# Optimization experiments

Hardware: AMD Instinct MI355X
Metric: run time of the kernel (lower is better)

Reference implementation:

```python
import jax, jax.numpy as jnp
import numpy as np

N = 100000
E = 1600000
E_PAIR = 100000
D_IN = 128
D_H = 128


def _sage_mean(x, src, dst, W_neigh, W_self, b):
    # DGL SAGEConv('mean'): out = fc_self(h_dst) + fc_neigh(mean_{u in N(v)} h_u) + bias
    n = x.shape[0]
    msg_sum = jax.ops.segment_sum(x[src], dst, num_segments=n)          # [N, d]
    deg = jax.ops.segment_sum(jnp.ones(src.shape, x.dtype), dst, num_segments=n)
    h_neigh = msg_sum / jnp.maximum(deg, 1.0)[:, None]
    return x @ W_self.T + h_neigh @ W_neigh.T + b


def setup_inputs() -> dict:
    key = jax.random.key(0)
    ks = jax.random.split(key, 16)
    def lin(k, fan_out, fan_in):
        s = 1.0 / np.sqrt(fan_in)
        return jax.random.uniform(k, (fan_out, fan_in), jnp.float32, -s, s)
    inp = {
        'x': jax.random.normal(ks[0], (N, D_IN), jnp.float32),
        'edge_src': jax.random.randint(ks[1], (E,), 0, N),
        'edge_dst': jax.random.randint(ks[2], (E,), 0, N),
        'pos_src': jax.random.randint(ks[3], (E_PAIR,), 0, N),
        'pos_dst': jax.random.randint(ks[4], (E_PAIR,), 0, N),
        'neg_src': jax.random.randint(ks[5], (E_PAIR,), 0, N),
        'neg_dst': jax.random.randint(ks[6], (E_PAIR,), 0, N),
        # SAGEConv layer 1 (in_feats -> n_hidden)
        'W1_neigh': lin(ks[7], D_H, D_IN),
        'W1_self': lin(ks[8], D_H, D_IN),
        'b1': jnp.zeros((D_H,), jnp.float32),
        # SAGEConv layer 2 (n_hidden -> n_hidden)
        'W2_neigh': lin(ks[9], D_H, D_H),
        'W2_self': lin(ks[10], D_H, D_H),
        'b2': jnp.zeros((D_H,), jnp.float32),
        # predictor MLP: Linear(2h->h) ReLU Linear(h->h) ReLU Linear(h->1)
        'P1_w': lin(ks[11], D_H, 2 * D_H),
        'P1_b': jnp.zeros((D_H,), jnp.float32),
        'P2_w': lin(ks[12], D_H, D_H),
        'P2_b': jnp.zeros((D_H,), jnp.float32),
        'P3_w': lin(ks[13], 1, D_H),
        'P3_b': jnp.zeros((1,), jnp.float32),
    }
    return inp


def _predict(h_src, h_dst, P1_w, P1_b, P2_w, P2_b, P3_w, P3_b):
    h = jnp.concatenate([h_src, h_dst], axis=1)
    h = jax.nn.relu(h @ P1_w.T + P1_b)
    h = jax.nn.relu(h @ P2_w.T + P2_b)
    return h @ P3_w.T + P3_b


def reference(x, edge_src, edge_dst, pos_src, pos_dst, neg_src, neg_dst,
              W1_neigh, W1_self, b1, W2_neigh, W2_self, b2,
              P1_w, P1_b, P2_w, P2_b, P3_w, P3_b):
    h = _sage_mean(x, edge_src, edge_dst, W1_neigh, W1_self, b1)
    h = jax.nn.relu(h)
    h = _sage_mean(h, edge_src, edge_dst, W2_neigh, W2_self, b2)
    h_pos = _predict(h[pos_src], h[pos_dst], P1_w, P1_b, P2_w, P2_b, P3_w, P3_b)
    h_neg = _predict(h[neg_src], h[neg_dst], P1_w, P1_b, P2_w, P2_b, P3_w, P3_b)
    return (h_pos, h_neg)
```

## Files before the change

### kernel.cpp

```cpp
#include <hip/hip_runtime.h>
#include <hip/hip_bf16.h>
#include <hip/hip_fp16.h>


#define D 128
#define NR 512
#define PART_CHUNK 4096
#define LDA 40
#define LDH2 136

typedef _Float16 f16x8 __attribute__((ext_vector_type(8)));
typedef float f32x4 __attribute__((ext_vector_type(4)));

__device__ __forceinline__ void cvt8(const float* src, _Float16* dst, int off8) {
    const float4* s4 = (const float4*)src;
    float4 a = s4[2 * off8], b = s4[2 * off8 + 1];
    f16x8 h;
    h[0] = (_Float16)a.x; h[1] = (_Float16)a.y; h[2] = (_Float16)a.z; h[3] = (_Float16)a.w;
    h[4] = (_Float16)b.x; h[5] = (_Float16)b.y; h[6] = (_Float16)b.z; h[7] = (_Float16)b.w;
    *(f16x8*)(dst + 8 * off8) = h;
}

__global__ __launch_bounds__(256) void k_setup(
    const float* __restrict__ x, _Float16* __restrict__ xf, int n8, int nb_x,
    const float* __restrict__ W1s, const float* __restrict__ W1n,
    const float* __restrict__ W2s, const float* __restrict__ W2n,
    const float* __restrict__ P1w, const float* __restrict__ P2w,
    _Float16* __restrict__ Ws1f, _Float16* __restrict__ Wn1f,
    _Float16* __restrict__ Ws2f, _Float16* __restrict__ Wn2f,
    _Float16* __restrict__ P1cf, _Float16* __restrict__ P2wf,
    const int* __restrict__ dst, int* __restrict__ region_cnt, int e, int bound) {
    int b = blockIdx.x;
    if (b < nb_x) {
        int i = b * 256 + threadIdx.x;
        if (i < n8) cvt8(x, xf, i);
        return;
    }
    b -= nb_x;
    if (b < 56) {
        int g = b * 256 + threadIdx.x;
        if (g >= 14336) return;
        if (g >= 8192 && g < 12288) {
            int u = g - 8192;
            int o = u >> 4, col = (u & 15) * 8;
            const float* src = P1w + (size_t)(o & 127) * 256 + ((o >> 7) * 128) + col;
            float4 a = *(const float4*)src, bb = *(const float4*)(src + 4);
            f16x8 h;
            h[0] = (_Float16)a.x; h[1] = (_Float16)a.y; h[2] = (_Float16)a.z; h[3] = (_Float16)a.w;
            h[4] = (_Float16)bb.x; h[5] = (_Float16)bb.y; h[6] = (_Float16)bb.z; h[7] = (_Float16)bb.w;
            *(f16x8*)(P1cf + (size_t)u * 8) = h;
            return;
        }
        const float* src; _Float16* dstp; int off;
        if      (g <  2048) { src = W1s; dstp = Ws1f; off = g; }
        else if (g <  4096) { src = W1n; dstp = Wn1f; off = g - 2048; }
        else if (g <  6144) { src = W2s; dstp = Ws2f; off = g - 4096; }
        else if (g <  8192) { src = W2n; dstp = Wn2f; off = g - 6144; }
        else                { src = P2w; dstp = P2wf; off = g - 12288; }
        cvt8(src, dstp, off);
        return;
    }
    b -= 56;
    __shared__ int s[NR];
    for (int i = threadIdx.x; i < NR; i += 256) s[i] = 0;
    __syncthreads();
    for (int i = b * 256 + threadIdx.x; i < e; i += 128 * 256)
        atomicAdd(&s[dst[i] / bound], 1);
    __syncthreads();
    for (int i = threadIdx.x; i < NR; i += 256)
        if (s[i]) atomicAdd(&region_cnt[i], s[i]);
}

__global__ void k_regbase(const int* __restrict__ region_cnt,
                          int* __restrict__ region_base, int* __restrict__ region_cursor) {
    if (threadIdx.x == 0 && blockIdx.x == 0) {
        int run = 0;
        for (int r = 0; r < NR; ++r) {
            region_base[r] = run; region_cursor[r] = run; run += region_cnt[r];
        }
        region_base[NR] = run;
    }
}

__global__ __launch_bounds__(256) void k_regpart(
    const int* __restrict__ src, const int* __restrict__ dst,
    unsigned int* __restrict__ eout, int* __restrict__ region_cursor, int e, int bound) {
    __shared__ int s_cnt[NR];
    __shared__ int s_base[NR];
    for (int c0 = blockIdx.x * PART_CHUNK; c0 < e; c0 += gridDim.x * PART_CHUNK) {
        int cend = min(c0 + PART_CHUNK, e);
        for (int i = threadIdx.x; i < NR; i += 256) s_cnt[i] = 0;
        __syncthreads();
        for (int i = c0 + threadIdx.x; i < cend; i += 256)
            atomicAdd(&s_cnt[dst[i] / bound], 1);
        __syncthreads();
        for (int i = threadIdx.x; i < NR; i += 256)
            s_base[i] = s_cnt[i] ? atomicAdd(&region_cursor[i], s_cnt[i]) : 0;
        __syncthreads();
        for (int i = threadIdx.x; i < NR; i += 256) s_cnt[i] = 0;
        __syncthreads();
        for (int i = c0 + threadIdx.x; i < cend; i += 256) {
            int d = dst[i];
            int r = d / bound;
            unsigned int doff = (unsigned int)(d - r * bound);
            int p = atomicAdd(&s_cnt[r], 1);
            eout[s_base[r] + p] = (unsigned int)src[i] | (doff << 20);
        }
        __syncthreads();
    }
}

#define EMAX 4608
__global__ __launch_bounds__(256) void k_rowoff_scatter(
    const unsigned int* __restrict__ ep, const int* __restrict__ region_base,
    int* __restrict__ row_off, int* __restrict__ csr, int n, int bound) {
    int r = blockIdx.x;
    int rlo = r * bound;
    if (threadIdx.x == 0 && r == 0) row_off[n] = region_base[NR];
    if (rlo >= n) return;
    int nn = min(bound, n - rlo);
    __shared__ unsigned int s_e[EMAX];
    __shared__ int s_deg[256];
    __shared__ int s_scan[256];
    __shared__ int s_cur[256];
    int beg = region_base[r], end = region_base[r + 1];
    int cnt = end - beg;
    bool fit = (cnt <= EMAX);
    if (fit)
        for (int i = threadIdx.x; i < cnt; i += 256) s_e[i] = ep[beg + i];
    s_deg[threadIdx.x] = 0;
    __syncthreads();
    for (int i = threadIdx.x; i < cnt; i += 256)
        atomicAdd(&s_deg[(fit ? s_e[i] : ep[beg + i]) >> 20], 1);
    __syncthreads();
    int v = (threadIdx.x < nn) ? s_deg[threadIdx.x] : 0;
    s_scan[threadIdx.x] = v;
    __syncthreads();
    #pragma unroll
    for (int off = 1; off < 256; off <<= 1) {
        int add = (threadIdx.x >= off) ? s_scan[threadIdx.x - off] : 0;
        __syncthreads();
        s_scan[threadIdx.x] += add;
        __syncthreads();
    }
    int base = beg + (threadIdx.x ? s_scan[threadIdx.x - 1] : 0);
    s_cur[threadIdx.x] = base;
    if (threadIdx.x < nn) row_off[rlo + threadIdx.x] = base;
    __syncthreads();
    for (int i = threadIdx.x; i < cnt; i += 256) {
        unsigned int e2 = fit ? s_e[i] : ep[beg + i];
        int doff = e2 >> 20;
        int p = atomicAdd(&s_cur[doff], 1);
        csr[p] = e2 & 0xFFFFF;
    }
}

__global__ __launch_bounds__(256) void k_agg(
    const _Float16* __restrict__ Xf, const int* __restrict__ row_off,
    const int* __restrict__ csr, _Float16* __restrict__ Aggf, int n_nodes) {
    int g = blockIdx.x * 16 + (threadIdx.x >> 4);
    if (g >= n_nodes) return;
    int l = threadIdx.x & 15;
    int beg = row_off[g], end = row_off[g + 1];
    float acc[8] = {0.f, 0.f, 0.f, 0.f, 0.f, 0.f, 0.f, 0.f};
    int i = beg;
    for (; i + 8 <= end; i += 8) {
        int si[8];
        #pragma unroll
        for (int j = 0; j < 8; ++j) si[j] = csr[i + j];
        f16x8 vv[8];
        #pragma unroll
        for (int j = 0; j < 8; ++j)
            vv[j] = *(const f16x8*)(Xf + (size_t)si[j] * D + l * 8);
        #pragma unroll
        for (int j = 0; j < 8; ++j)
            #pragma unroll
            for (int k = 0; k < 8; ++k) acc[k] += (float)vv[j][k];
    }
    for (; i + 2 <= end; i += 2) {
        int s0 = csr[i], s1 = csr[i + 1];
        f16x8 v0 = *(const f16x8*)(Xf + (size_t)s0 * D + l * 8);
        f16x8 v1 = *(const f16x8*)(Xf + (size_t)s1 * D + l * 8);
        #pragma unroll
        for (int k = 0; k < 8; ++k) acc[k] += (float)v0[k] + (float)v1[k];
    }
    if (i < end) {
        int s0 = csr[i];
        f16x8 v0 = *(const f16x8*)(Xf + (size_t)s0 * D + l * 8);
        #pragma unroll
        for (int k = 0; k < 8; ++k) acc[k] += (float)v0[k];
    }
    float inv = 1.0f / fmaxf((float)(end - beg), 1.0f);
    f16x8 o;
    #pragma unroll
    for (int k = 0; k < 8; ++k) o[k] = (_Float16)(acc[k] * inv);
    *(f16x8*)(Aggf + (size_t)g * D + l * 8) = o;
}

__global__ __launch_bounds__(512) void k_transform(
    const _Float16* __restrict__ Xf, const _Float16* __restrict__ Aggf,
    const _Float16* __restrict__ Wsf, const _Float16* __restrict__ Wnf,
    const float* __restrict__ bias, _Float16* __restrict__ outf,
    int n_rows, int do_relu) {
    __shared__ _Float16 s_a[2][128 * LDA];
    __shared__ _Float16 s_b[2][128 * LDA];
    int tid = threadIdx.x;
    int w = tid >> 6, l = tid & 63;
    int wr = w >> 1, wc = w & 1;
    int l15 = l & 15, lk = l >> 4;
    int n0 = blockIdx.x * 128;
    int r = tid >> 2, q = tid & 3;
    int rstage = n0 + r; if (rstage >= n_rows) rstage = n_rows - 1;

    f32x4 acc[2][4];
    #pragma unroll
    for (int i = 0; i < 2; ++i)
        #pragma unroll
        for (int j = 0; j < 4; ++j) acc[i][j] = (f32x4){0.f, 0.f, 0.f, 0.f};

    int a_off = (wr * 32 + l15) * LDA + lk * 8;
    int b_off = (wc * 64 + l15) * LDA + lk * 8;
    int st_off = r * LDA + q * 8;

    {
        f16x8 av = *(const f16x8*)(Xf + (size_t)rstage * D + q * 8);
        f16x8 wv = *(const f16x8*)(Wsf + (size_t)r * D + q * 8);
        *(f16x8*)(&s_a[0][st_off]) = av;
        *(f16x8*)(&s_b[0][st_off]) = wv;
    }
    __syncthreads();

    for (int c = 0; c < 8; ++c) {
        int b = c & 1;
        f16x8 av, wv;
        if (c < 7) {
            int cn = c + 1;
            const _Float16* asrc = (cn < 4) ? Xf : Aggf;
            const _Float16* wsrc = (cn < 4) ? Wsf : Wnf;
            int kb = (cn & 3) * 32;
            av = *(const f16x8*)(asrc + (size_t)rstage * D + kb + q * 8);
            wv = *(const f16x8*)(wsrc + (size_t)r * D + kb + q * 8);
        }
        f16x8 af[2], bf[4];
        af[0] = *(const f16x8*)(&s_a[b][a_off]);
        af[1] = *(const f16x8*)(&s_a[b][a_off + 16 * LDA]);
        #pragma unroll
        for (int j = 0; j < 4; ++j) bf[j] = *(const f16x8*)(&s_b[b][b_off + j * 16 * LDA]);
        #pragma unroll
        for (int i = 0; i < 2; ++i)
            #pragma unroll
            for (int j = 0; j < 4; ++j)
                acc[i][j] = __builtin_amdgcn_mfma_f32_16x16x32_f16(af[i], bf[j], acc[i][j], 0, 0, 0);
        if (c < 7) {
            *(f16x8*)(&s_a[b ^ 1][st_off]) = av;
            *(f16x8*)(&s_b[b ^ 1][st_off]) = wv;
        }
        __syncthreads();
    }

    #pragma unroll
    for (int j = 0; j < 4; ++j) {
        int col = wc * 64 + j * 16 + l15;
        float bv = bias[col];
        #pragma unroll
        for (int i = 0; i < 2; ++i) {
            int rowb = n0 + wr * 32 + i * 16 + lk * 4;
            #pragma unroll
            for (int v = 0; v < 4; ++v) {
                int row = rowb + v;
                if (row < n_rows) {
                    float xv = acc[i][j][v] + bv;
                    if (do_relu) xv = fmaxf(xv, 0.f);
                    outf[(size_t)row * D + col] = (_Float16)xv;
                }
            }
        }
    }
}

__global__ __launch_bounds__(512) void k_pre(
    const _Float16* __restrict__ Hf, const _Float16* __restrict__ P1cf,
    _Float16* __restrict__ Pre, int n_rows) {
    __shared__ _Float16 s_a[64 * LDA];
    __shared__ _Float16 s_b[256 * LDA];
    int tid = threadIdx.x;
    int w = tid >> 6, l = tid & 63;
    int wr = w >> 2, wc = w & 3;
    int l15 = l & 15, lk = l >> 4;
    int n0 = blockIdx.x * 64;

    f32x4 acc[2][4];
    #pragma unroll
    for (int i = 0; i < 2; ++i)
        #pragma unroll
        for (int j = 0; j < 4; ++j) acc[i][j] = (f32x4){0.f, 0.f, 0.f, 0.f};

    int a_off = (wr * 32 + l15) * LDA + lk * 8;

    for (int c = 0; c < 4; ++c) {
        int kb = c * 32;
        __syncthreads();
        if (tid < 256) {
            int r = tid >> 2, q = tid & 3;
            int rstage = n0 + r; if (rstage >= n_rows) rstage = n_rows - 1;
            *(f16x8*)(&s_a[r * LDA + q * 8]) =
                *(const f16x8*)(Hf + (size_t)rstage * D + kb + q * 8);
        }
        #pragma unroll
        for (int e = 0; e < 2; ++e) {
            int idx = tid + e * 512;
            int o = idx >> 2, q = idx & 3;
            *(f16x8*)(&s_b[o * LDA + q * 8]) =
                *(const f16x8*)(P1cf + (size_t)o * 128 + kb + q * 8);
        }
        __syncthreads();
        f16x8 af[2], bf[4];
        af[0] = *(const f16x8*)(&s_a[a_off]);
        af[1] = *(const f16x8*)(&s_a[a_off + 16 * LDA]);
        #pragma unroll
        for (int j = 0; j < 4; ++j)
            bf[j] = *(const f16x8*)(&s_b[(wc * 64 + j * 16 + l15) * LDA + lk * 8]);
        #pragma unroll
        for (int i = 0; i < 2; ++i)
            #pragma unroll
            for (int j = 0; j < 4; ++j)
                acc[i][j] = __builtin_amdgcn_mfma_f32_16x16x32_f16(af[i], bf[j], acc[i][j], 0, 0, 0);
    }

    #pragma unroll
    for (int j = 0; j < 4; ++j) {
        int col = wc * 64 + j * 16 + l15;
        #pragma unroll
        for (int i = 0; i < 2; ++i) {
            int rowb = n0 + wr * 32 + i * 16 + lk * 4;
            #pragma unroll
            for (int v = 0; v < 4; ++v) {
                int row = rowb + v;
                if (row < n_rows)
                    Pre[(size_t)row * 256 + col] = (_Float16)acc[i][j][v];
            }
        }
    }
}

__global__ __launch_bounds__(256) void k_mlp(
    const _Float16* __restrict__ Pre,
    const int* __restrict__ pos_src, const int* __restrict__ pos_dst,
    const int* __restrict__ neg_src, const int* __restrict__ neg_dst,
    const float* __restrict__ P1b,
    const _Float16* __restrict__ P2wf, const float* __restrict__ P2b,
    const float* __restrict__ P3w, const float* __restrict__ P3b,
    float* __restrict__ out, int EP) {
    __shared__ _Float16 s_h1[64 * LDH2];
    __shared__ _Float16 s_b[2][128 * LDA];
    __shared__ float s_red[64 * 2];
    __shared__ int s_node[128];
    int tid = threadIdx.x;
    int w = tid >> 6, l = tid & 63;
    int wr = w >> 1, wc = w & 1;
    int l15 = l & 15, lk = l >> 4;
    int p0 = blockIdx.x * 64;
    int twoEP = 2 * EP;

    if (tid < 128) {
        int p = p0 + (tid & 63);
        if (p >= twoEP) p = twoEP - 1;
        int node;
        if (tid < 64) node = (p < EP) ? pos_src[p] : neg_src[p - EP];
        else          node = (p < EP) ? pos_dst[p] : neg_dst[p - EP];
        s_node[tid] = node;
    }
    __syncthreads();

    #pragma unroll
    for (int e = 0; e < 4; ++e) {
        int idx = tid + e * 256;
        int pr = idx >> 4, u = idx & 15;
        int sn = s_node[pr], dn = s_node[64 + pr];
        f16x8 a = *(const f16x8*)(Pre + (size_t)sn * 256 + u * 8);
        f16x8 b = *(const f16x8*)(Pre + (size_t)dn * 256 + 128 + u * 8);
        float4 b0 = *(const float4*)(P1b + u * 8);
        float4 b1 = *(const float4*)(P1b + u * 8 + 4);
        float bb[8] = {b0.x, b0.y, b0.z, b0.w, b1.x, b1.y, b1.z, b1.w};
        f16x8 h;
        #pragma unroll
        for (int j = 0; j < 8; ++j)
            h[j] = (_Float16)fmaxf((float)a[j] + (float)b[j] + bb[j], 0.f);
        *(f16x8*)(&s_h1[pr * LDH2 + u * 8]) = h;
    }
    #pragma unroll
    for (int e = 0; e < 2; ++e) {
        int idx = tid + e * 256;
        int o = idx >> 2, q = idx & 3;
        *(f16x8*)(&s_b[0][o * LDA + q * 8]) = *(const f16x8*)(P2wf + (size_t)o * D + q * 8);
    }
    __syncthreads();

    f32x4 acc2[2][4];
    #pragma unroll
    for (int i = 0; i < 2; ++i)
        #pragma unroll
        for (int j = 0; j < 4; ++j) acc2[i][j] = (f32x4){0.f, 0.f, 0.f, 0.f};

    for (int c = 0; c < 4; ++c) {
        int b = c & 1;
        f16x8 nw[2];
        if (c < 3) {
            #pragma unroll
            for (int e = 0; e < 2; ++e) {
                int idx = tid + e * 256;
                int o = idx >> 2, q = idx & 3;
                nw[e] = *(const f16x8*)(P2wf + (size_t)o * D + (c + 1) * 32 + q * 8);
            }
        }
        f16x8 af[2], bf[4];
        af[0] = *(const f16x8*)(&s_h1[(wr * 32 + l15) * LDH2 + c * 32 + lk * 8]);
        af[1] = *(const f16x8*)(&s_h1[(wr * 32 + 16 + l15) * LDH2 + c * 32 + lk * 8]);
        #pragma unroll
        for (int j = 0; j < 4; ++j)
            bf[j] = *(const f16x8*)(&s_b[b][(wc * 64 + j * 16 + l15) * LDA + lk * 8]);
        #pragma unroll
        for (int i = 0; i < 2; ++i)
            #pragma unroll
            for (int j = 0; j < 4; ++j)
                acc2[i][j] = __builtin_amdgcn_mfma_f32_16x16x32_f16(af[i], bf[j], acc2[i][j], 0, 0, 0);
        if (c < 3) {
            #pragma unroll
            for (int e = 0; e < 2; ++e) {
                int idx = tid + e * 256;
                int o = idx >> 2, q = idx & 3;
                *(f16x8*)(&s_b[b ^ 1][o * LDA + q * 8]) = nw[e];
            }
        }
        __syncthreads();
    }

    float b2v[4], pw[4];
    #pragma unroll
    for (int j = 0; j < 4; ++j) {
        int col = wc * 64 + j * 16 + l15;
        b2v[j] = P2b[col];
        pw[j] = P3w[col];
    }
    #pragma unroll
    for (int i = 0; i < 2; ++i) {
        #pragma unroll
        for (int v = 0; v < 4; ++v) {
            float s = 0.f;
            #pragma unroll
            for (int j = 0; j < 4; ++j)
                s += fmaxf(acc2[i][j][v] + b2v[j], 0.f) * pw[j];
            s += __shfl_xor(s, 1);
            s += __shfl_xor(s, 2);
            s += __shfl_xor(s, 4);
            s += __shfl_xor(s, 8);
            if (l15 == 0)
                s_red[(wr * 32 + i * 16 + lk * 4 + v) * 2 + wc] = s;
        }
    }
    __syncthreads();
    if (tid < 64) {
        int p = p0 + tid;
        if (p < twoEP) out[p] = s_red[tid * 2] + s_red[tid * 2 + 1] + P3b[0];
    }
}

static inline size_t align_up(size_t x, size_t a) { return (x + a - 1) & ~(a - 1); }

extern "C" void kernel_launch(void* const* d_in, const int* in_sizes, int n_in,
                              void* d_out, int out_size, void* d_ws, size_t ws_size,
                              hipStream_t stream) {
    const float* x        = (const float*)d_in[0];
    const int*   edge_src = (const int*)d_in[1];
    const int*   edge_dst = (const int*)d_in[2];
    const int*   pos_src  = (const int*)d_in[3];
    const int*   pos_dst  = (const int*)d_in[4];
    const int*   neg_src  = (const int*)d_in[5];
    const int*   neg_dst  = (const int*)d_in[6];
    const float* W1n = (const float*)d_in[7];
    const float* W1s = (const float*)d_in[8];
    const float* b1  = (const float*)d_in[9];
    const float* W2n = (const float*)d_in[10];
    const float* W2s = (const float*)d_in[11];
    const float* b2  = (const float*)d_in[12];
    const float* P1w = (const float*)d_in[13];
    const float* P1b = (const float*)d_in[14];
    const float* P2w = (const float*)d_in[15];
    const float* P2b = (const float*)d_in[16];
    const float* P3w = (const float*)d_in[17];
    const float* P3b = (const float*)d_in[18];
    float* out = (float*)d_out;

    const int N = in_sizes[0] / D;
    const int E = in_sizes[1];
    const int EP = in_sizes[3];
    const int bound = (N + NR - 1) / NR;

    char* ws = (char*)d_ws;
    size_t off = 0;
    int* row_off = (int*)(ws + off); off = align_up(off + (size_t)(N + 1) * 4, 256);
    int* regmeta = (int*)(ws + off); off = align_up(off + (size_t)(3 * NR + 8) * 4, 256);
    int* csr     = (int*)(ws + off); off = align_up(off + (size_t)E * 4, 256);
    unsigned int* epart = (unsigned int*)(ws + off); off = align_up(off + (size_t)E * 4, 256);
    _Float16* xf   = (_Float16*)(ws + off); off = align_up(off + (size_t)N * D * 2, 256);
    _Float16* aggf = (_Float16*)(ws + off); off = align_up(off + (size_t)N * D * 2, 256);
    _Float16* h1f  = (_Float16*)(ws + off); off = align_up(off + (size_t)N * D * 2, 256);
    _Float16* h2f  = (_Float16*)(ws + off); off = align_up(off + (size_t)N * D * 2, 256);
    _Float16* Ws1f = (_Float16*)(ws + off); off = align_up(off + (size_t)D * D * 2, 256);
    _Float16* Wn1f = (_Float16*)(ws + off); off = align_up(off + (size_t)D * D * 2, 256);
    _Float16* Ws2f = (_Float16*)(ws + off); off = align_up(off + (size_t)D * D * 2, 256);
    _Float16* Wn2f = (_Float16*)(ws + off); off = align_up(off + (size_t)D * D * 2, 256);
    _Float16* P1cf = (_Float16*)(ws + off); off = align_up(off + (size_t)2 * D * D * 2, 256);
    _Float16* P2wf = (_Float16*)(ws + off); off = align_up(off + (size_t)D * D * 2, 256);
    (void)ws_size;

    _Float16* Pre = xf;

    int* region_cnt    = regmeta;
    int* region_base   = regmeta + NR;
    int* region_cursor = regmeta + 2 * NR + 4;

    const int n8 = N * D / 8;
    const int nb_x = (n8 + 255) / 256;

    hipMemsetAsync(region_cnt, 0, NR * 4, stream);
    k_setup<<<nb_x + 56 + 128, 256, 0, stream>>>(
        x, xf, n8, nb_x, W1s, W1n, W2s, W2n, P1w, P2w,
        Ws1f, Wn1f, Ws2f, Wn2f, P1cf, P2wf,
        edge_dst, region_cnt, E, bound);
    k_regbase<<<1, 1, 0, stream>>>(region_cnt, region_base, region_cursor);
    k_regpart<<<(E + PART_CHUNK - 1) / PART_CHUNK, 256, 0, stream>>>(
        edge_src, edge_dst, epart, region_cursor, E, bound);
    k_rowoff_scatter<<<NR, 256, 0, stream>>>(epart, region_base, row_off, csr, N, bound);

    const int ngrid = (N + 127) / 128;
    const int pgrid = (2 * EP + 63) / 64;

    k_agg<<<(N + 15) / 16, 256, 0, stream>>>(xf, row_off, csr, aggf, N);
    k_transform<<<ngrid, 512, 0, stream>>>(xf, aggf, Ws1f, Wn1f, b1, h1f, N, 1);
    k_agg<<<(N + 15) / 16, 256, 0, stream>>>(h1f, row_off, csr, aggf, N);
    k_transform<<<ngrid, 512, 0, stream>>>(h1f, aggf, Ws2f, Wn2f, b2, h2f, N, 0);

    k_pre<<<(N + 63) / 64, 512, 0, stream>>>(h2f, P1cf, Pre, N);
    k_mlp<<<pgrid, 256, 0, stream>>>(Pre, pos_src, pos_dst, neg_src, neg_dst,
                                     P1b, P2wf, P2b, P3w, P3b, out, EP);
}
```

Before: 310.3 us.

## Fuse layer-2 transform with predictor pre-projection; parallelize region scan and partition

The second SAGE transform now keeps its output tile in shared memory and immediately multiplies it by the predictor's first-layer weights, so the h2 intermediate is never written to or re-read from global memory and one kernel launch goes away. The single-thread region prefix sum becomes a 512-thread shared-memory scan. The edge partition kernel switches to a fixed grid of 128 blocks, each owning one contiguous slice, which cuts the number of global cursor atomics. The fused kernel uses more shared memory (an extra 128x136 half tile), which may lower occupancy.

```diff
diff --git a/kernel.cpp b/kernel.cpp
--- a/kernel.cpp
+++ b/kernel.cpp
@@ -5,8 +5,8 @@
 
 #define D 128
 #define NR 512
-#define PART_CHUNK 4096
 #define LDA 40
+#define LDAGG 136
 #define LDH2 136
 
 typedef _Float16 f16x8 __attribute__((ext_vector_type(8)));
@@ -71,15 +71,25 @@
         if (s[i]) atomicAdd(&region_cnt[i], s[i]);
 }
 
-__global__ void k_regbase(const int* __restrict__ region_cnt,
-                          int* __restrict__ region_base, int* __restrict__ region_cursor) {
-    if (threadIdx.x == 0 && blockIdx.x == 0) {
-        int run = 0;
-        for (int r = 0; r < NR; ++r) {
-            region_base[r] = run; region_cursor[r] = run; run += region_cnt[r];
-        }
-        region_base[NR] = run;
-    }
+__global__ __launch_bounds__(NR) void k_regbase(
+    const int* __restrict__ region_cnt,
+    int* __restrict__ region_base, int* __restrict__ region_cursor) {
+    __shared__ int s[NR];
+    int t = threadIdx.x;
+    int v = region_cnt[t];
+    s[t] = v;
+    __syncthreads();
+    #pragma unroll
+    for (int off = 1; off < NR; off <<= 1) {
+        int add = (t >= off) ? s[t - off] : 0;
+        __syncthreads();
+        s[t] += add;
+        __syncthreads();
+    }
+    int ex = s[t] - v;
+    region_base[t] = ex;
+    region_cursor[t] = ex;
+    if (t == NR - 1) region_base[NR] = s[t];
 }
 
 __global__ __launch_bounds__(256) void k_regpart(
@@ -87,26 +97,25 @@
     unsigned int* __restrict__ eout, int* __restrict__ region_cursor, int e, int bound) {
     __shared__ int s_cnt[NR];
     __shared__ int s_base[NR];
-    for (int c0 = blockIdx.x * PART_CHUNK; c0 < e; c0 += gridDim.x * PART_CHUNK) {
-        int cend = min(c0 + PART_CHUNK, e);
-        for (int i = threadIdx.x; i < NR; i += 256) s_cnt[i] = 0;
-        __syncthreads();
-        for (int i = c0 + threadIdx.x; i < cend; i += 256)
-            atomicAdd(&s_cnt[dst[i] / bound], 1);
-        __syncthreads();
-        for (int i = threadIdx.x; i < NR; i += 256)
-            s_base[i] = s_cnt[i] ? atomicAdd(&region_cursor[i], s_cnt[i]) : 0;
-        __syncthreads();
-        for (int i = threadIdx.x; i < NR; i += 256) s_cnt[i] = 0;
-        __syncthreads();
-        for (int i = c0 + threadIdx.x; i < cend; i += 256) {
-            int d = dst[i];
-            int r = d / bound;
-            unsigned int doff = (unsigned int)(d - r * bound);
-            int p = atomicAdd(&s_cnt[r], 1);
-            eout[s_base[r] + p] = (unsigned int)src[i] | (doff << 20);
-        }
-        __syncthreads();
+    int per = (e + gridDim.x - 1) / gridDim.x;
+    int beg = blockIdx.x * per;
+    int end = min(beg + per, e);
+    for (int i = threadIdx.x; i < NR; i += 256) s_cnt[i] = 0;
+    __syncthreads();
+    for (int i = beg + threadIdx.x; i < end; i += 256)
+        atomicAdd(&s_cnt[dst[i] / bound], 1);
+    __syncthreads();
+    for (int i = threadIdx.x; i < NR; i += 256)
+        s_base[i] = s_cnt[i] ? atomicAdd(&region_cursor[i], s_cnt[i]) : 0;
+    __syncthreads();
+    for (int i = threadIdx.x; i < NR; i += 256) s_cnt[i] = 0;
+    __syncthreads();
+    for (int i = beg + threadIdx.x; i < end; i += 256) {
+        int d = dst[i];
+        int r = d / bound;
+        unsigned int doff = (unsigned int)(d - r * bound);
+        int p = atomicAdd(&s_cnt[r], 1);
+        eout[s_base[r] + p] = (unsigned int)src[i] | (doff << 20);
     }
 }
 
@@ -200,8 +209,7 @@
 __global__ __launch_bounds__(512) void k_transform(
     const _Float16* __restrict__ Xf, const _Float16* __restrict__ Aggf,
     const _Float16* __restrict__ Wsf, const _Float16* __restrict__ Wnf,
-    const float* __restrict__ bias, _Float16* __restrict__ outf,
-    int n_rows, int do_relu) {
+    const float* __restrict__ bias, _Float16* __restrict__ outf, int n_rows) {
     __shared__ _Float16 s_a[2][128 * LDA];
     __shared__ _Float16 s_b[2][128 * LDA];
     int tid = threadIdx.x;
@@ -268,76 +276,133 @@
             #pragma unroll
             for (int v = 0; v < 4; ++v) {
                 int row = rowb + v;
-                if (row < n_rows) {
-                    float xv = acc[i][j][v] + bv;
-                    if (do_relu) xv = fmaxf(xv, 0.f);
-                    outf[(size_t)row * D + col] = (_Float16)xv;
-                }
-            }
-        }
-    }
-}
-
-__global__ __launch_bounds__(512) void k_pre(
-    const _Float16* __restrict__ Hf, const _Float16* __restrict__ P1cf,
+                if (row < n_rows)
+                    outf[(size_t)row * D + col] = (_Float16)fmaxf(acc[i][j][v] + bv, 0.f);
+            }
+        }
+    }
+}
+
+__global__ __launch_bounds__(512) void k_transform_pre(
+    const _Float16* __restrict__ Xf, const _Float16* __restrict__ Aggf,
+    const _Float16* __restrict__ Wsf, const _Float16* __restrict__ Wnf,
+    const float* __restrict__ bias, const _Float16* __restrict__ P1cf,
     _Float16* __restrict__ Pre, int n_rows) {
-    __shared__ _Float16 s_a[64 * LDA];
-    __shared__ _Float16 s_b[256 * LDA];
+    __shared__ _Float16 s_a[2][128 * LDA];
+    __shared__ _Float16 s_b[2][128 * LDA];
+    __shared__ _Float16 s_h2[128 * LDAGG];
     int tid = threadIdx.x;
     int w = tid >> 6, l = tid & 63;
-    int wr = w >> 2, wc = w & 3;
     int l15 = l & 15, lk = l >> 4;
-    int n0 = blockIdx.x * 64;
-
-    f32x4 acc[2][4];
-    #pragma unroll
-    for (int i = 0; i < 2; ++i)
-        #pragma unroll
-        for (int j = 0; j < 4; ++j) acc[i][j] = (f32x4){0.f, 0.f, 0.f, 0.f};
-
-    int a_off = (wr * 32 + l15) * LDA + lk * 8;
-
-    for (int c = 0; c < 4; ++c) {
-        int kb = c * 32;
+    int n0 = blockIdx.x * 128;
+    int r = tid >> 2, q = tid & 3;
+    int rstage = n0 + r; if (rstage >= n_rows) rstage = n_rows - 1;
+
+    {
+        int wr = w >> 1, wc = w & 1;
+        f32x4 acc[2][4];
+        #pragma unroll
+        for (int i = 0; i < 2; ++i)
+            #pragma unroll
+            for (int j = 0; j < 4; ++j) acc[i][j] = (f32x4){0.f, 0.f, 0.f, 0.f};
+
+        int a_off = (wr * 32 + l15) * LDA + lk * 8;
+        int b_off = (wc * 64 + l15) * LDA + lk * 8;
+        int st_off = r * LDA + q * 8;
+
+        f16x8 av0 = *(const f16x8*)(Xf + (size_t)rstage * D + q * 8);
+        f16x8 wv0 = *(const f16x8*)(Wsf + (size_t)r * D + q * 8);
+        *(f16x8*)(&s_a[0][st_off]) = av0;
+        *(f16x8*)(&s_b[0][st_off]) = wv0;
         __syncthreads();
-        if (tid < 256) {
-            int r = tid >> 2, q = tid & 3;
-            int rstage = n0 + r; if (rstage >= n_rows) rstage = n_rows - 1;
-            *(f16x8*)(&s_a[r * LDA + q * 8]) =
-                *(const f16x8*)(Hf + (size_t)rstage * D + kb + q * 8);
-        }
-        #pragma unroll
-        for (int e = 0; e < 2; ++e) {
-            int idx = tid + e * 512;
-            int o = idx >> 2, q = idx & 3;
-            *(f16x8*)(&s_b[o * LDA + q * 8]) =
-                *(const f16x8*)(P1cf + (size_t)o * 128 + kb + q * 8);
-        }
-        __syncthreads();
-        f16x8 af[2], bf[4];
-        af[0] = *(const f16x8*)(&s_a[a_off]);
-        af[1] = *(const f16x8*)(&s_a[a_off + 16 * LDA]);
-        #pragma unroll
-        for (int j = 0; j < 4; ++j)
-            bf[j] = *(const f16x8*)(&s_b[(wc * 64 + j * 16 + l15) * LDA + lk * 8]);
-        #pragma unroll
-        for (int i = 0; i < 2; ++i)
+
+        for (int c = 0; c < 8; ++c) {
+            int b = c & 1;
+            f16x8 av, wv;
+            if (c < 7) {
+                int cn = c + 1;
+                const _Float16* asrc = (cn < 4) ? Xf : Aggf;
+                const _Float16* wsrc = (cn < 4) ? Wsf : Wnf;
+                int kb = (cn & 3) * 32;
+                av = *(const f16x8*)(asrc + (size_t)rstage * D + kb + q * 8);
+                wv = *(const f16x8*)(wsrc + (size_t)r * D + kb + q * 8);
+            }
+            f16x8 af[2], bf[4];
+            af[0] = *(const f16x8*)(&s_a[b][a_off]);
+            af[1] = *(const f16x8*)(&s_a[b][a_off + 16 * LDA]);
+            #pragma unroll
+            for (int j = 0; j < 4; ++j) bf[j] = *(const f16x8*)(&s_b[b][b_off + j * 16 * LDA]);
+            #pragma unroll
+            for (int i = 0; i < 2; ++i)
+                #pragma unroll
+                for (int j = 0; j < 4; ++j)
+                    acc[i][j] = __builtin_amdgcn_mfma_f32_16x16x32_f16(af[i], bf[j], acc[i][j], 0, 0, 0);
+            if (c < 7) {
+                *(f16x8*)(&s_a[b ^ 1][st_off]) = av;
+                *(f16x8*)(&s_b[b ^ 1][st_off]) = wv;
+            }
+            __syncthreads();
+        }
+
+        #pragma unroll
+        for (int j = 0; j < 4; ++j) {
+            int col = wc * 64 + j * 16 + l15;
+            float bv = bias[col];
+            #pragma unroll
+            for (int i = 0; i < 2; ++i) {
+                int rowb = wr * 32 + i * 16 + lk * 4;
+                #pragma unroll
+                for (int v = 0; v < 4; ++v)
+                    s_h2[(rowb + v) * LDAGG + col] = (_Float16)(acc[i][j][v] + bv);
+            }
+        }
+    }
+
+    {
+        int wr = w >> 2, wc = w & 3;
+        _Float16* s_flat = &s_a[0][0];
+        f32x4 acc2[4][4];
+        #pragma unroll
+        for (int i = 0; i < 4; ++i)
+            #pragma unroll
+            for (int j = 0; j < 4; ++j) acc2[i][j] = (f32x4){0.f, 0.f, 0.f, 0.f};
+
+        for (int c2 = 0; c2 < 4; ++c2) {
+            __syncthreads();
+            #pragma unroll
+            for (int e = 0; e < 2; ++e) {
+                int idx = tid + e * 512;
+                int o = idx >> 2, qq = idx & 3;
+                *(f16x8*)(&s_flat[o * LDA + qq * 8]) =
+                    *(const f16x8*)(P1cf + (size_t)o * 128 + c2 * 32 + qq * 8);
+            }
+            __syncthreads();
+            f16x8 af[4], bf[4];
+            #pragma unroll
+            for (int i = 0; i < 4; ++i)
+                af[i] = *(const f16x8*)(&s_h2[(wr * 64 + i * 16 + l15) * LDAGG + c2 * 32 + lk * 8]);
             #pragma unroll
             for (int j = 0; j < 4; ++j)
-                acc[i][j] = __builtin_amdgcn_mfma_f32_16x16x32_f16(af[i], bf[j], acc[i][j], 0, 0, 0);
-    }
-
-    #pragma unroll
-    for (int j = 0; j < 4; ++j) {
-        int col = wc * 64 + j * 16 + l15;
-        #pragma unroll
-        for (int i = 0; i < 2; ++i) {
-            int rowb = n0 + wr * 32 + i * 16 + lk * 4;
-            #pragma unroll
-            for (int v = 0; v < 4; ++v) {
-                int row = rowb + v;
-                if (row < n_rows)
-                    Pre[(size_t)row * 256 + col] = (_Float16)acc[i][j][v];
+                bf[j] = *(const f16x8*)(&s_flat[(wc * 64 + j * 16 + l15) * LDA + lk * 8]);
+            #pragma unroll
+            for (int i = 0; i < 4; ++i)
+                #pragma unroll
+                for (int j = 0; j < 4; ++j)
+                    acc2[i][j] = __builtin_amdgcn_mfma_f32_16x16x32_f16(af[i], bf[j], acc2[i][j], 0, 0, 0);
+        }
+
+        #pragma unroll
+        for (int j = 0; j < 4; ++j) {
+            int col = wc * 64 + j * 16 + l15;
+            #pragma unroll
+            for (int i = 0; i < 4; ++i) {
+                int rowb = n0 + wr * 64 + i * 16 + lk * 4;
+                #pragma unroll
+                for (int v = 0; v < 4; ++v) {
+                    int row = rowb + v;
+                    if (row < n_rows)
+                        Pre[(size_t)row * 256 + col] = (_Float16)acc2[i][j][v];
+                }
             }
         }
     }
@@ -505,7 +570,7 @@
     _Float16* xf   = (_Float16*)(ws + off); off = align_up(off + (size_t)N * D * 2, 256);
     _Float16* aggf = (_Float16*)(ws + off); off = align_up(off + (size_t)N * D * 2, 256);
     _Float16* h1f  = (_Float16*)(ws + off); off = align_up(off + (size_t)N * D * 2, 256);
-    _Float16* h2f  = (_Float16*)(ws + off); off = align_up(off + (size_t)N * D * 2, 256);
+    _Float16* Pre  = (_Float16*)(ws + off); off = align_up(off + (size_t)N * 256 * 2, 256);
     _Float16* Ws1f = (_Float16*)(ws + off); off = align_up(off + (size_t)D * D * 2, 256);
     _Float16* Wn1f = (_Float16*)(ws + off); off = align_up(off + (size_t)D * D * 2, 256);
     _Float16* Ws2f = (_Float16*)(ws + off); off = align_up(off + (size_t)D * D * 2, 256);
@@ -514,8 +579,6 @@
     _Float16* P2wf = (_Float16*)(ws + off); off = align_up(off + (size_t)D * D * 2, 256);
     (void)ws_size;
 
-    _Float16* Pre = xf;
-
     int* region_cnt    = regmeta;
     int* region_base   = regmeta + NR;
     int* region_cursor = regmeta + 2 * NR + 4;
@@ -528,20 +591,18 @@
         x, xf, n8, nb_x, W1s, W1n, W2s, W2n, P1w, P2w,
         Ws1f, Wn1f, Ws2f, Wn2f, P1cf, P2wf,
         edge_dst, region_cnt, E, bound);
-    k_regbase<<<1, 1, 0, stream>>>(region_cnt, region_base, region_cursor);
-    k_regpart<<<(E + PART_CHUNK - 1) / PART_CHUNK, 256, 0, stream>>>(
-        edge_src, edge_dst, epart, region_cursor, E, bound);
+    k_regbase<<<1, NR, 0, stream>>>(region_cnt, region_base, region_cursor);
+    k_regpart<<<128, 256, 0, stream>>>(edge_src, edge_dst, epart, region_cursor, E, bound);
     k_rowoff_scatter<<<NR, 256, 0, stream>>>(epart, region_base, row_off, csr, N, bound);
 
     const int ngrid = (N + 127) / 128;
     const int pgrid = (2 * EP + 63) / 64;
 
     k_agg<<<(N + 15) / 16, 256, 0, stream>>>(xf, row_off, csr, aggf, N);
-    k_transform<<<ngrid, 512, 0, stream>>>(xf, aggf, Ws1f, Wn1f, b1, h1f, N, 1);
+    k_transform<<<ngrid, 512, 0, stream>>>(xf, aggf, Ws1f, Wn1f, b1, h1f, N);
     k_agg<<<(N + 15) / 16, 256, 0, stream>>>(h1f, row_off, csr, aggf, N);
-    k_transform<<<ngrid, 512, 0, stream>>>(h1f, aggf, Ws2f, Wn2f, b2, h2f, N, 0);
-
-    k_pre<<<(N + 63) / 64, 512, 0, stream>>>(h2f, P1cf, Pre, N);
+    k_transform_pre<<<ngrid, 512, 0, stream>>>(h1f, aggf, Ws2f, Wn2f, b2, P1cf, Pre, N);
+
     k_mlp<<<pgrid, 256, 0, stream>>>(Pre, pos_src, pos_dst, neg_src, neg_dst,
                                      P1b, P2wf, P2b, P3w, P3b, out, EP);
 }
```

Result: faster. 303.5 us (median of 2 runs) (-2.2%).
